# Kernel optimization log

Measured on AMD Instinct MI355X. Metric: run time of the kernel, lower is better.

Reference implementation:

```python
import jax, jax.numpy as jnp
import numpy as np

L, D, F, H, K, V, E = 15, 512, 2048, 64, 128, 30, 1024
DH = D // H  # 8
B, N = 8, 128


def _ln(x, s, b, eps=1e-5):
    m = x.mean(-1, keepdims=True)
    v = ((x - m) ** 2).mean(-1, keepdims=True)
    return (x - m) * jax.lax.rsqrt(v + eps) * s + b


def _gauss(x, mean, std):
    # matches torch.jit gaussian(): pi = 3.14159
    a = (2.0 * 3.14159) ** 0.5
    return jnp.exp(-0.5 * ((x - mean) / std) ** 2) / (a * std)


def setup_inputs() -> dict:
    key = jax.random.key(0)
    ks = iter(jax.random.split(key, 48))
    nrm = lambda shape, sc=0.02: jax.random.normal(next(ks), shape, jnp.float32) * sc
    zeros = lambda shape: jnp.zeros(shape, jnp.float32)
    ones = lambda shape: jnp.ones(shape, jnp.float32)
    return dict(
        src_tokens=jax.random.randint(next(ks), (B, N), 0, V),
        src_distance=jax.random.uniform(next(ks), (B, N, N), jnp.float32) * 3.0,
        src_edge_type=jax.random.randint(next(ks), (B, N, N), 0, E),
        token_embed=nrm((V, D)),
        gbf_means=jax.random.uniform(next(ks), (K,), jnp.float32, 0.0, 3.0),
        gbf_stds=jax.random.uniform(next(ks), (K,), jnp.float32, 0.0, 3.0),
        gbf_mul=ones((E, 1)),
        gbf_bias=zeros((E, 1)),
        proj_w1=nrm((K, K)), proj_b1=zeros((K,)),
        proj_w2=nrm((K, H)), proj_b2=zeros((H,)),
        emb_ln_s=ones((D,)), emb_ln_b=zeros((D,)),
        Wq=nrm((L, D, D)), bq=zeros((L, D)),
        Wk=nrm((L, D, D)), bk=zeros((L, D)),
        Wv=nrm((L, D, D)), bv=zeros((L, D)),
        Wo=nrm((L, D, D)), bo=zeros((L, D)),
        ln1_s=ones((L, D)), ln1_b=zeros((L, D)),
        ln2_s=ones((L, D)), ln2_b=zeros((L, D)),
        Wf1=nrm((L, D, F)), bf1=zeros((L, F)),
        Wf2=nrm((L, F, D)), bf2=zeros((L, D)),
        fin_ln_s=ones((D,)), fin_ln_b=zeros((D,)),
    )


def reference(src_tokens, src_distance, src_edge_type, token_embed,
              gbf_means, gbf_stds, gbf_mul, gbf_bias,
              proj_w1, proj_b1, proj_w2, proj_b2,
              emb_ln_s, emb_ln_b,
              Wq, bq, Wk, bk, Wv, bv, Wo, bo,
              ln1_s, ln1_b, ln2_s, ln2_b,
              Wf1, bf1, Wf2, bf2, fin_ln_s, fin_ln_b):
    # --- GaussianLayer: per-pair edge-type affine + K-kernel RBF -> [B,N,N,K]
    mul = gbf_mul[src_edge_type]          # [B,N,N,1]
    add = gbf_bias[src_edge_type]         # [B,N,N,1]
    g = mul * src_distance[..., None] + add
    std = jnp.abs(gbf_stds) + 1e-5
    g = _gauss(g, gbf_means, std)         # broadcast [B,N,N,1] vs [K] -> [B,N,N,K]
    # --- gbf_proj (NonLinearHead K->K->H) -> attention bias [B,H,N,N]
    hproj = jax.nn.gelu(g @ proj_w1 + proj_b1, approximate=False)
    bias0 = jnp.transpose(hproj @ proj_w2 + proj_b2, (0, 3, 1, 2))

    x = _ln(token_embed[src_tokens], emb_ln_s, emb_ln_b)  # [B,N,D]
    scale = DH ** -0.5

    def layer(carry, p):
        x, bias = carry
        wq, bq_, wk, bk_, wv, bv_, wo, bo_, s1, b1, s2, b2, wf1, bf1_, wf2, bf2_ = p
        # pre-LN self-attention with additive pair bias
        r = x
        y = _ln(x, s1, b1)
        q = (y @ wq + bq_).reshape(B, N, H, DH) * scale
        k = (y @ wk + bk_).reshape(B, N, H, DH)
        v = (y @ wv + bv_).reshape(B, N, H, DH)
        scores = jnp.einsum('bihd,bjhd->bhij', q, k) + bias  # [B,H,N,N]
        probs = jax.nn.softmax(scores, axis=-1)
        o = jnp.einsum('bhij,bjhd->bihd', probs, v).reshape(B, N, D)
        x = r + (o @ wo + bo_)
        # pre-LN FFN
        r = x
        y = _ln(x, s2, b2)
        y = jax.nn.gelu(y @ wf1 + bf1_, approximate=False) @ wf2 + bf2_
        # UniMol: pre-softmax scores feed the next layer as its pair bias
        return (r + y, scores), None

    (x, _), _ = jax.lax.scan(
        layer, (x, bias0),
        (Wq, bq, Wk, bk, Wv, bv, Wo, bo, ln1_s, ln1_b, ln2_s, ln2_b, Wf1, bf1, Wf2, bf2))
    return _ln(x, fin_ln_s, fin_ln_b)  # [B,N,D]
```

## Files before the change

kernel.cpp:

```cpp
#include <hip/hip_runtime.h>
#include <hip/hip_bf16.h>

#define Bv 8
#define Nv 128
#define Dv 512
#define Hv 64
#define DHv 8
#define Fv 2048
#define Lv 15
#define Kv 128

typedef unsigned short u16;
typedef __attribute__((ext_vector_type(8))) short s16x8;
typedef __attribute__((ext_vector_type(4))) float f32x4;

__device__ __forceinline__ float b2f(u16 u) {
    union { unsigned int i; float f; } w;
    w.i = ((unsigned int)u) << 16;
    return w.f;
}

__device__ __forceinline__ u16 f2b(float f) {
    __hip_bfloat16 h = __float2bfloat16(f);
    u16 u;
    __builtin_memcpy(&u, &h, 2);
    return u;
}

__device__ __forceinline__ bool probe_bf16(const void* p) {
    return ((const u16*)p)[0] == 0x3F80u;
}

__device__ __forceinline__ float ldv(const u16* p, size_t i)   { return b2f(p[i]); }
__device__ __forceinline__ float ldv(const float* p, size_t i) { return p[i]; }

__device__ __forceinline__ u16 ld16(const u16* p, size_t i)   { return p[i]; }
__device__ __forceinline__ u16 ld16(const float* p, size_t i) { return f2b(p[i]); }

__device__ __forceinline__ float geluf(float v) {
    return 0.5f * v * (1.0f + erff(v * 0.70710678118654752f));
}

template<typename T>
__device__ __forceinline__ void gbf2_body(
    const T* dist, const int* etype, const T* means, const T* stds,
    const T* mulW, const T* addW, const T* w1, const T* b1w,
    const T* w2, const T* b2w, float* biasOut,
    float* xs, float* smean, float* sinv, u16* GA, u16* Bst)
{
    const int t = threadIdx.x;
    const int iq = blockIdx.x;
    const int j0 = blockIdx.y << 6;
    const int b = blockIdx.z;

    if (t < 64) {
        size_t pidx = ((size_t)(b * Nv + iq)) * Nv + j0 + t;
        int e = etype[pidx];
        xs[t] = ldv(dist, pidx) * ldv(mulW, e) + ldv(addW, e);
    } else if (t >= 128) {
        int k = t - 128;
        float sv = fabsf(ldv(stds, k)) + 1e-5f;
        smean[k] = ldv(means, k);
        sinv[k] = 1.0f / sv;
    }
    __syncthreads();

    {
        const int row = t & 63;
        const int kc = t >> 6;
        const float x = xs[row];
        const int mt = row >> 4, r = row & 15;
        #pragma unroll
        for (int lg2 = 0; lg2 < 4; lg2++) {
            union { s16x8 v; u16 u[8]; } pk;
            #pragma unroll
            for (int j = 0; j < 8; j++) {
                int k = kc * 32 + lg2 * 8 + j;
                float z = (x - smean[k]) * sinv[k];
                pk.u[j] = f2b(expf(-0.5f * z * z) * (0.39894261f * sinv[k]));
            }
            *reinterpret_cast<s16x8*>(&GA[(((mt * 4 + kc) * 4 + lg2) * 16 + r) << 3]) = pk.v;
        }
    }

    const int w = t >> 6, l = t & 63;
    const int lg = l >> 4, lr = l & 15;
    const int wm = (w >> 1) << 5;
    const int wn1 = (w & 1) << 6;
    const int mt0 = wm >> 4;

    const int b1col = t & 127, b1lg0 = (t >> 7) << 1;

    f32x4 acc1[2][4];
    #pragma unroll
    for (int mi = 0; mi < 2; mi++)
        #pragma unroll
        for (int ni = 0; ni < 4; ni++) acc1[mi][ni] = (f32x4){0.f, 0.f, 0.f, 0.f};

    for (int kc = 0; kc < 4; kc++) {
        #pragma unroll
        for (int q = 0; q < 2; q++) {
            int lgq = b1lg0 + q;
            union { s16x8 v; u16 u[8]; } pb;
            #pragma unroll
            for (int j = 0; j < 8; j++)
                pb.u[j] = ld16(w1, (size_t)(kc * 32 + lgq * 8 + j) * Kv + b1col);
            *reinterpret_cast<s16x8*>(
                &Bst[((((b1col >> 4) * 4 + lgq) * 16 + (b1col & 15)) << 3)]) = pb.v;
        }
        __syncthreads();
        s16x8 a0 = *reinterpret_cast<const s16x8*>(&GA[((((mt0 + 0) * 4 + kc) * 4 + lg) * 16 + lr) << 3]);
        s16x8 a1 = *reinterpret_cast<const s16x8*>(&GA[((((mt0 + 1) * 4 + kc) * 4 + lg) * 16 + lr) << 3]);
        #pragma unroll
        for (int ni = 0; ni < 4; ni++) {
            int nt = (wn1 >> 4) + ni;
            s16x8 bf = *reinterpret_cast<const s16x8*>(&Bst[((nt * 4 + lg) * 16 + lr) << 3]);
            acc1[0][ni] = __builtin_amdgcn_mfma_f32_16x16x32_bf16(a0, bf, acc1[0][ni], 0, 0, 0);
            acc1[1][ni] = __builtin_amdgcn_mfma_f32_16x16x32_bf16(a1, bf, acc1[1][ni], 0, 0, 0);
        }
        __syncthreads();
    }

    #pragma unroll
    for (int mi = 0; mi < 2; mi++) {
        #pragma unroll
        for (int ni = 0; ni < 4; ni++) {
            int col = wn1 + ni * 16 + lr;
            float bb = ldv(b1w, col);
            #pragma unroll
            for (int i = 0; i < 4; i++) {
                int row = wm + mi * 16 + lg * 4 + i;
                float v = geluf(acc1[mi][ni][i] + bb);
                GA[((((row >> 4) * 4 + (col >> 5)) * 4 + ((col >> 3) & 3)) * 16 + (row & 15)) * 8 + (col & 7)] = f2b(v);
            }
        }
    }
    __syncthreads();

    const int wn2 = (w & 1) << 5;
    const int b2col = t & 63, b2lg = t >> 6;

    f32x4 acc2[2][2];
    #pragma unroll
    for (int mi = 0; mi < 2; mi++)
        #pragma unroll
        for (int ni = 0; ni < 2; ni++) acc2[mi][ni] = (f32x4){0.f, 0.f, 0.f, 0.f};

    for (int kc = 0; kc < 4; kc++) {
        {
            union { s16x8 v; u16 u[8]; } pb;
            #pragma unroll
            for (int j = 0; j < 8; j++)
                pb.u[j] = ld16(w2, (size_t)(kc * 32 + b2lg * 8 + j) * Hv + b2col);
            *reinterpret_cast<s16x8*>(
                &Bst[((((b2col >> 4) * 4 + b2lg) * 16 + (b2col & 15)) << 3)]) = pb.v;
        }
        __syncthreads();
        s16x8 a0 = *reinterpret_cast<const s16x8*>(&GA[((((mt0 + 0) * 4 + kc) * 4 + lg) * 16 + lr) << 3]);
        s16x8 a1 = *reinterpret_cast<const s16x8*>(&GA[((((mt0 + 1) * 4 + kc) * 4 + lg) * 16 + lr) << 3]);
        #pragma unroll
        for (int ni = 0; ni < 2; ni++) {
            int nt = (wn2 >> 4) + ni;
            s16x8 bf = *reinterpret_cast<const s16x8*>(&Bst[((nt * 4 + lg) * 16 + lr) << 3]);
            acc2[0][ni] = __builtin_amdgcn_mfma_f32_16x16x32_bf16(a0, bf, acc2[0][ni], 0, 0, 0);
            acc2[1][ni] = __builtin_amdgcn_mfma_f32_16x16x32_bf16(a1, bf, acc2[1][ni], 0, 0, 0);
        }
        __syncthreads();
    }

    #pragma unroll
    for (int mi = 0; mi < 2; mi++) {
        #pragma unroll
        for (int ni = 0; ni < 2; ni++) {
            int h = wn2 + ni * 16 + lr;
            int jb = wm + mi * 16 + lg * 4;
            float badd = ldv(b2w, h);
            size_t oidx = (((size_t)(b * Hv + h)) * Nv + iq) * Nv + j0 + jb;
            *reinterpret_cast<float4*>(&biasOut[oidx]) =
                make_float4(acc2[mi][ni][0] + badd, acc2[mi][ni][1] + badd,
                            acc2[mi][ni][2] + badd, acc2[mi][ni][3] + badd);
        }
    }
}

__global__ __launch_bounds__(256) void gbf2_k(
    const void* dist, const int* etype, const void* means, const void* stds,
    const void* mulW, const void* addW, const void* w1, const void* b1,
    const void* w2, const void* b2, float* biasOut, const void* probe)
{
    __shared__ float xs[64];
    __shared__ float smean[Kv];
    __shared__ float sinv[Kv];
    __shared__ __align__(16) u16 GA[8192];
    __shared__ __align__(16) u16 Bst[4096];
    if (probe_bf16(probe))
        gbf2_body<u16>((const u16*)dist, etype, (const u16*)means, (const u16*)stds,
                       (const u16*)mulW, (const u16*)addW, (const u16*)w1, (const u16*)b1,
                       (const u16*)w2, (const u16*)b2, biasOut, xs, smean, sinv, GA, Bst);
    else
        gbf2_body<float>((const float*)dist, etype, (const float*)means, (const float*)stds,
                         (const float*)mulW, (const float*)addW, (const float*)w1, (const float*)b1,
                         (const float*)w2, (const float*)b2, biasOut, xs, smean, sinv, GA, Bst);
}

__device__ __forceinline__ void block_stats_512(float x0, float x1, float& mean, float& rstd)
{
    float sum = x0 + x1, sq = x0 * x0 + x1 * x1;
    #pragma unroll
    for (int off = 32; off; off >>= 1) {
        sum += __shfl_xor(sum, off);
        sq  += __shfl_xor(sq, off);
    }
    __shared__ float ssum[4], ssq[4];
    int t = threadIdx.x;
    if ((t & 63) == 0) { ssum[t >> 6] = sum; ssq[t >> 6] = sq; }
    __syncthreads();
    sum = ssum[0] + ssum[1] + ssum[2] + ssum[3];
    sq  = ssq[0] + ssq[1] + ssq[2] + ssq[3];
    mean = sum * (1.0f / 512.0f);
    float var = sq * (1.0f / 512.0f) - mean * mean;
    rstd = rsqrtf(var + 1e-5f);
}

template<typename T>
__device__ __forceinline__ void embed_body(
    const int* toks, const T* emb, const T* sc, const T* bi, float* xout)
{
    int row = blockIdx.x, t = threadIdx.x;
    int tok = toks[row];
    float x0 = ldv(emb, (size_t)tok * Dv + t);
    float x1 = ldv(emb, (size_t)tok * Dv + t + 256);
    float mean, rstd;
    block_stats_512(x0, x1, mean, rstd);
    xout[(size_t)row * Dv + t]       = (x0 - mean) * rstd * ldv(sc, t) + ldv(bi, t);
    xout[(size_t)row * Dv + t + 256] = (x1 - mean) * rstd * ldv(sc, t + 256) + ldv(bi, t + 256);
}

__global__ __launch_bounds__(256) void embed_ln_k(
    const int* toks, const void* emb, const void* sc, const void* bi,
    float* xout, const void* probe)
{
    if (probe_bf16(probe))
        embed_body<u16>(toks, (const u16*)emb, (const u16*)sc, (const u16*)bi, xout);
    else
        embed_body<float>(toks, (const float*)emb, (const float*)sc, (const float*)bi, xout);
}

template<typename T>
__device__ __forceinline__ void ln_body(
    const float* xin, const T* sc, const T* bi, size_t pofs, float* yout)
{
    int row = blockIdx.x, t = threadIdx.x;
    const float* xp = xin + (size_t)row * Dv;
    float x0 = xp[t], x1 = xp[t + 256];
    float mean, rstd;
    block_stats_512(x0, x1, mean, rstd);
    yout[(size_t)row * Dv + t]       = (x0 - mean) * rstd * ldv(sc, pofs + t) + ldv(bi, pofs + t);
    yout[(size_t)row * Dv + t + 256] = (x1 - mean) * rstd * ldv(sc, pofs + t + 256) + ldv(bi, pofs + t + 256);
}

__global__ __launch_bounds__(256) void ln_k(
    const float* xin, const void* sc, const void* bi, unsigned long long pofs,
    float* yout, const void* probe)
{
    if (probe_bf16(probe))
        ln_body<u16>(xin, (const u16*)sc, (const u16*)bi, (size_t)pofs, yout);
    else
        ln_body<float>(xin, (const float*)sc, (const float*)bi, (size_t)pofs, yout);
}

template<typename T, bool OUT_BF>
__device__ __forceinline__ void final_ln_body(
    const float* xin, const T* sc, const T* bi, void* yout)
{
    int row = blockIdx.x, t = threadIdx.x;
    const float* xp = xin + (size_t)row * Dv;
    float x0 = xp[t], x1 = xp[t + 256];
    float mean, rstd;
    block_stats_512(x0, x1, mean, rstd);
    float o0 = (x0 - mean) * rstd * ldv(sc, t) + ldv(bi, t);
    float o1 = (x1 - mean) * rstd * ldv(sc, t + 256) + ldv(bi, t + 256);
    if (OUT_BF) {
        __hip_bfloat16* yp = (__hip_bfloat16*)yout;
        yp[(size_t)row * Dv + t]       = __float2bfloat16(o0);
        yp[(size_t)row * Dv + t + 256] = __float2bfloat16(o1);
    } else {
        float* yp = (float*)yout;
        yp[(size_t)row * Dv + t]       = o0;
        yp[(size_t)row * Dv + t + 256] = o1;
    }
}

__global__ __launch_bounds__(256) void final_ln_k(
    const float* xin, const void* sc, const void* bi, void* yout, const void* probe)
{
    if (probe_bf16(probe))
        final_ln_body<u16, true>(xin, (const u16*)sc, (const u16*)bi, yout);
    else
        final_ln_body<float, false>(xin, (const float*)sc, (const float*)bi, yout);
}

template<typename T>
__device__ __forceinline__ void gemm_mfma_body(
    const float* A, const T* W, const T* bias, const float* R,
    float* C, int Nc, int Kc, int act, int res, int kbegin, int kend, int raw,
    u16* Al, u16* Bl)
{
    const int tid = threadIdx.x;
    const int l = tid & 63, w = tid >> 6;
    const int wm = (w >> 1) << 5, wn = (w & 1) << 5;
    const int bm = blockIdx.y * 64, bn = blockIdx.x * 64;
    const int lg = l >> 4, lr = l & 15;
    const int mt0 = wm >> 4, nt0 = wn >> 4;

    f32x4 acc00 = {}, acc01 = {}, acc10 = {}, acc11 = {};

    const int arow = tid >> 2, akq = tid & 3;
    const float* aGp = A + (size_t)(bm + arow) * Kc + (akq << 3);
    const int aL0 = ((((arow >> 4) * 2 + 0) * 4 + akq) * 16 + (arow & 15)) << 3;
    const int aL1 = ((((arow >> 4) * 2 + 1) * 4 + akq) * 16 + (arow & 15)) << 3;

    const int bcol = tid & 63;
    const int be = tid >> 6;
    const int bc = be >> 1, blg0 = (be & 1) << 1;
    const int bnt = bcol >> 4, bcl = bcol & 15;

    for (int kt = kbegin; kt < kend; kt += 64) {
        {
            float4 a0 = *reinterpret_cast<const float4*>(aGp + kt);
            float4 a1 = *reinterpret_cast<const float4*>(aGp + kt + 4);
            float4 a2 = *reinterpret_cast<const float4*>(aGp + kt + 32);
            float4 a3 = *reinterpret_cast<const float4*>(aGp + kt + 36);
            union { s16x8 v; u16 u[8]; } p0, p1;
            p0.u[0] = f2b(a0.x); p0.u[1] = f2b(a0.y); p0.u[2] = f2b(a0.z); p0.u[3] = f2b(a0.w);
            p0.u[4] = f2b(a1.x); p0.u[5] = f2b(a1.y); p0.u[6] = f2b(a1.z); p0.u[7] = f2b(a1.w);
            p1.u[0] = f2b(a2.x); p1.u[1] = f2b(a2.y); p1.u[2] = f2b(a2.z); p1.u[3] = f2b(a2.w);
            p1.u[4] = f2b(a3.x); p1.u[5] = f2b(a3.y); p1.u[6] = f2b(a3.z); p1.u[7] = f2b(a3.w);
            *reinterpret_cast<s16x8*>(&Al[aL0]) = p0.v;
            *reinterpret_cast<s16x8*>(&Al[aL1]) = p1.v;
        }
        #pragma unroll
        for (int q = 0; q < 2; q++) {
            int lgq = blg0 + q;
            union { s16x8 v; u16 u[8]; } pb;
            #pragma unroll
            for (int j = 0; j < 8; j++)
                pb.u[j] = ld16(W, (size_t)(kt + bc * 32 + lgq * 8 + j) * Nc + bn + bcol);
            *reinterpret_cast<s16x8*>(
                &Bl[(((bnt * 2 + bc) * 4 + lgq) * 16 + bcl) << 3]) = pb.v;
        }
        __syncthreads();
        #pragma unroll
        for (int c = 0; c < 2; c++) {
            s16x8 af0 = *reinterpret_cast<const s16x8*>(&Al[((((mt0 + 0) * 2 + c) * 4 + lg) * 16 + lr) << 3]);
            s16x8 af1 = *reinterpret_cast<const s16x8*>(&Al[((((mt0 + 1) * 2 + c) * 4 + lg) * 16 + lr) << 3]);
            s16x8 bf0 = *reinterpret_cast<const s16x8*>(&Bl[((((nt0 + 0) * 2 + c) * 4 + lg) * 16 + lr) << 3]);
            s16x8 bf1 = *reinterpret_cast<const s16x8*>(&Bl[((((nt0 + 1) * 2 + c) * 4 + lg) * 16 + lr) << 3]);
            acc00 = __builtin_amdgcn_mfma_f32_16x16x32_bf16(af0, bf0, acc00, 0, 0, 0);
            acc01 = __builtin_amdgcn_mfma_f32_16x16x32_bf16(af0, bf1, acc01, 0, 0, 0);
            acc10 = __builtin_amdgcn_mfma_f32_16x16x32_bf16(af1, bf0, acc10, 0, 0, 0);
            acc11 = __builtin_amdgcn_mfma_f32_16x16x32_bf16(af1, bf1, acc11, 0, 0, 0);
        }
        __syncthreads();
    }

    #pragma unroll
    for (int mi = 0; mi < 2; mi++) {
        #pragma unroll
        for (int i = 0; i < 4; i++) {
            const int row = bm + wm + mi * 16 + lg * 4 + i;
            float* Crow = C + (size_t)row * Nc;
            const float* Rrow = res ? (R + (size_t)row * Nc) : nullptr;
            #pragma unroll
            for (int ni = 0; ni < 2; ni++) {
                const int col = bn + wn + ni * 16 + lr;
                float cv = (ni == 0) ? (mi == 0 ? acc00[i] : acc10[i])
                                     : (mi == 0 ? acc01[i] : acc11[i]);
                if (!raw) {
                    cv += ldv(bias, col);
                    if (act) cv = geluf(cv);
                    if (res) cv += Rrow[col];
                }
                Crow[col] = cv;
            }
        }
    }
}

__global__ __launch_bounds__(256) void gemm_k(
    const float* A, const void* W, unsigned long long wofs,
    const void* bias, unsigned long long bofs, const float* R,
    float* C, int Nc, int Kc, int act, int res, const void* probe)
{
    __shared__ __align__(16) u16 Al[4096];
    __shared__ __align__(16) u16 Bl[4096];
    const int nz = gridDim.z, z = blockIdx.z;
    const int kchunk = Kc / nz;
    const int kbegin = z * kchunk, kend = kbegin + kchunk;
    const int raw = (nz > 1) ? 1 : 0;
    float* Cz = C + (size_t)z * ((size_t)gridDim.y * 64) * Nc;
    if (probe_bf16(probe))
        gemm_mfma_body<u16>(A, (const u16*)W + wofs, (const u16*)bias + bofs, R, Cz,
                            Nc, Kc, act, res, kbegin, kend, raw, Al, Bl);
    else
        gemm_mfma_body<float>(A, (const float*)W + wofs, (const float*)bias + bofs, R, Cz,
                              Nc, Kc, act, res, kbegin, kend, raw, Al, Bl);
}

__global__ __launch_bounds__(256) void qkv_k(
    const float* A,
    const void* W0, const void* W1p, const void* W2p, unsigned long long wofs,
    const void* b0, const void* b1p, const void* b2p, unsigned long long bofs,
    float* C0, float* C1, float* C2, const void* probe)
{
    __shared__ __align__(16) u16 Al[4096];
    __shared__ __align__(16) u16 Bl[4096];
    const int z = blockIdx.z;
    const void* W  = (z == 0) ? W0 : (z == 1) ? W1p : W2p;
    const void* bb = (z == 0) ? b0 : (z == 1) ? b1p : b2p;
    float* C       = (z == 0) ? C0 : (z == 1) ? C1 : C2;
    if (probe_bf16(probe))
        gemm_mfma_body<u16>(A, (const u16*)W + wofs, (const u16*)bb + bofs, nullptr, C,
                            Dv, Dv, 0, 0, 0, Dv, 0, Al, Bl);
    else
        gemm_mfma_body<float>(A, (const float*)W + wofs, (const float*)bb + bofs, nullptr, C,
                              Dv, Dv, 0, 0, 0, Dv, 0, Al, Bl);
}

template<typename T>
__device__ __forceinline__ void combln_body(
    const float* parts, const T* pbias, float* X,
    const T* lnS, const T* lnB, size_t pofs, float* Y)
{
    const int t = threadIdx.x;
    const int rowb = t >> 7;
    const int col = (t & 127) << 2;
    const int row = (blockIdx.x << 1) + rowb;
    const size_t idx = (size_t)row * Dv + col;

    float4 sv = *reinterpret_cast<const float4*>(&parts[idx]);
    #pragma unroll
    for (int p = 1; p < 4; p++) {
        const float4 q2 = *reinterpret_cast<const float4*>(&parts[(size_t)p * 524288 + idx]);
        sv.x += q2.x; sv.y += q2.y; sv.z += q2.z; sv.w += q2.w;
    }
    sv.x += ldv(pbias, col);     sv.y += ldv(pbias, col + 1);
    sv.z += ldv(pbias, col + 2); sv.w += ldv(pbias, col + 3);
    const float4 r = *reinterpret_cast<const float4*>(&X[idx]);
    sv.x += r.x; sv.y += r.y; sv.z += r.z; sv.w += r.w;
    *reinterpret_cast<float4*>(&X[idx]) = sv;

    float sum = sv.x + sv.y + sv.z + sv.w;
    float sq  = sv.x * sv.x + sv.y * sv.y + sv.z * sv.z + sv.w * sv.w;
    #pragma unroll
    for (int off = 32; off; off >>= 1) {
        sum += __shfl_xor(sum, off);
        sq  += __shfl_xor(sq, off);
    }
    __shared__ float ssum[4], ssq[4];
    const int wv = t >> 6;
    if ((t & 63) == 0) { ssum[wv] = sum; ssq[wv] = sq; }
    __syncthreads();
    sum = ssum[rowb * 2] + ssum[rowb * 2 + 1];
    sq  = ssq[rowb * 2] + ssq[rowb * 2 + 1];
    const float mean = sum * (1.0f / 512.0f);
    const float var = sq * (1.0f / 512.0f) - mean * mean;
    const float rstd = rsqrtf(var + 1e-5f);

    float4 yv;
    yv.x = (sv.x - mean) * rstd * ldv(lnS, pofs + col)     + ldv(lnB, pofs + col);
    yv.y = (sv.y - mean) * rstd * ldv(lnS, pofs + col + 1) + ldv(lnB, pofs + col + 1);
    yv.z = (sv.z - mean) * rstd * ldv(lnS, pofs + col + 2) + ldv(lnB, pofs + col + 2);
    yv.w = (sv.w - mean) * rstd * ldv(lnS, pofs + col + 3) + ldv(lnB, pofs + col + 3);
    *reinterpret_cast<float4*>(&Y[idx]) = yv;
}

__global__ __launch_bounds__(256) void combln_k(
    const float* parts, const void* pbias, unsigned long long bofs, float* X,
    const void* lnS, const void* lnB, unsigned long long pofs, float* Y,
    const void* probe)
{
    if (probe_bf16(probe))
        combln_body<u16>(parts, (const u16*)pbias + bofs, X,
                         (const u16*)lnS, (const u16*)lnB, (size_t)pofs, Y);
    else
        combln_body<float>(parts, (const float*)pbias + bofs, X,
                           (const float*)lnS, (const float*)lnB, (size_t)pofs, Y);
}

__global__ __launch_bounds__(512) void attn_k(
    const float* __restrict__ q, const float* __restrict__ k, const float* __restrict__ v,
    float* bias, float* __restrict__ o)
{
    __shared__ __align__(16) float ks[Nv][DHv];
    __shared__ __align__(16) float vs[Nv][DHv];

    const int t = threadIdx.x;
    const int h = blockIdx.x;
    const int b = blockIdx.y;
    const int i = (blockIdx.z << 6) + (t >> 3);
    const int e = t & 7;
    const float scale = 0.35355339059327373f;

    const float* kh = k + (size_t)(b * Nv) * Dv + h * DHv;
    const float* vh = v + (size_t)(b * Nv) * Dv + h * DHv;

    {
        const int j = t >> 2, c = (t & 3) << 1;
        const float2 k2 = *reinterpret_cast<const float2*>(kh + (size_t)j * Dv + c);
        const float2 v2 = *reinterpret_cast<const float2*>(vh + (size_t)j * Dv + c);
        *reinterpret_cast<float2*>(&ks[j][c]) = k2;
        *reinterpret_cast<float2*>(&vs[j][c]) = v2;
    }

    const float* qp = q + (size_t)(b * Nv + i) * Dv + h * DHv;
    const float4 q0 = *reinterpret_cast<const float4*>(qp);
    const float4 q1 = *reinterpret_cast<const float4*>(qp + 4);

    float* bp = bias + (((size_t)(b * Hv + h)) * Nv + i) * Nv;

    float s[16];
    #pragma unroll
    for (int w = 0; w < 16; w++) s[w] = bp[(w << 3) + e];

    __syncthreads();

    float mx = -1e30f;
    #pragma unroll
    for (int w = 0; w < 16; w++) {
        const int j = (w << 3) + e;
        const float4 k0 = *reinterpret_cast<const float4*>(&ks[j][0]);
        const float4 k1 = *reinterpret_cast<const float4*>(&ks[j][4]);
        float d = q0.x * k0.x + q0.y * k0.y + q0.z * k0.z + q0.w * k0.w +
                  q1.x * k1.x + q1.y * k1.y + q1.z * k1.z + q1.w * k1.w;
        float val = s[w] + scale * d;
        s[w] = val;
        bp[j] = val;
        mx = fmaxf(mx, val);
    }

    mx = fmaxf(mx, __shfl_xor(mx, 1));
    mx = fmaxf(mx, __shfl_xor(mx, 2));
    mx = fmaxf(mx, __shfl_xor(mx, 4));

    float sum = 0.0f;
    #pragma unroll
    for (int w = 0; w < 16; w++) {
        s[w] = expf(s[w] - mx);
        sum += s[w];
    }
    sum += __shfl_xor(sum, 1);
    sum += __shfl_xor(sum, 2);
    sum += __shfl_xor(sum, 4);
    const float inv = 1.0f / sum;

    float a0 = 0, a1 = 0, a2 = 0, a3 = 0, a4 = 0, a5 = 0, a6 = 0, a7 = 0;
    #pragma unroll
    for (int w = 0; w < 16; w++) {
        const int j = (w << 3) + e;
        const float4 v0 = *reinterpret_cast<const float4*>(&vs[j][0]);
        const float4 v1 = *reinterpret_cast<const float4*>(&vs[j][4]);
        const float p = s[w];
        a0 += p * v0.x; a1 += p * v0.y; a2 += p * v0.z; a3 += p * v0.w;
        a4 += p * v1.x; a5 += p * v1.y; a6 += p * v1.z; a7 += p * v1.w;
    }
    a0 += __shfl_xor(a0, 1); a0 += __shfl_xor(a0, 2); a0 += __shfl_xor(a0, 4);
    a1 += __shfl_xor(a1, 1); a1 += __shfl_xor(a1, 2); a1 += __shfl_xor(a1, 4);
    a2 += __shfl_xor(a2, 1); a2 += __shfl_xor(a2, 2); a2 += __shfl_xor(a2, 4);
    a3 += __shfl_xor(a3, 1); a3 += __shfl_xor(a3, 2); a3 += __shfl_xor(a3, 4);
    a4 += __shfl_xor(a4, 1); a4 += __shfl_xor(a4, 2); a4 += __shfl_xor(a4, 4);
    a5 += __shfl_xor(a5, 1); a5 += __shfl_xor(a5, 2); a5 += __shfl_xor(a5, 4);
    a6 += __shfl_xor(a6, 1); a6 += __shfl_xor(a6, 2); a6 += __shfl_xor(a6, 4);
    a7 += __shfl_xor(a7, 1); a7 += __shfl_xor(a7, 2); a7 += __shfl_xor(a7, 4);

    if (e == 0) {
        float* op = o + (size_t)(b * Nv + i) * Dv + h * DHv;
        *reinterpret_cast<float4*>(op)     = make_float4(a0 * inv, a1 * inv, a2 * inv, a3 * inv);
        *reinterpret_cast<float4*>(op + 4) = make_float4(a4 * inv, a5 * inv, a6 * inv, a7 * inv);
    }
}

extern "C" void kernel_launch(void* const* d_in, const int* in_sizes, int n_in,
                              void* d_out, int out_size, void* d_ws, size_t ws_size,
                              hipStream_t stream)
{
    const int*  src_tokens = (const int*)d_in[0];
    const void* src_dist   = d_in[1];
    const int*  src_edge   = (const int*)d_in[2];
    const void* token_emb  = d_in[3];
    const void* gbf_means  = d_in[4];
    const void* gbf_stds   = d_in[5];
    const void* gbf_mul    = d_in[6];
    const void* gbf_bias   = d_in[7];
    const void* pw1        = d_in[8];
    const void* pb1        = d_in[9];
    const void* pw2        = d_in[10];
    const void* pb2        = d_in[11];
    const void* embs       = d_in[12];
    const void* embb       = d_in[13];
    const void* Wq         = d_in[14];
    const void* bq         = d_in[15];
    const void* Wk         = d_in[16];
    const void* bk         = d_in[17];
    const void* Wv         = d_in[18];
    const void* bvp        = d_in[19];
    const void* Wo         = d_in[20];
    const void* bo         = d_in[21];
    const void* ln1s       = d_in[22];
    const void* ln1b       = d_in[23];
    const void* ln2s       = d_in[24];
    const void* ln2b       = d_in[25];
    const void* Wf1        = d_in[26];
    const void* bf1        = d_in[27];
    const void* Wf2        = d_in[28];
    const void* bf2        = d_in[29];
    const void* fins       = d_in[30];
    const void* finb       = d_in[31];
    const void* probe      = embs;

    float* ws   = (float*)d_ws;
    float* x    = ws;
    float* y    = x  + 524288;
    float* qb   = y  + 524288;
    float* kb   = qb + 524288;
    float* vb   = kb + 524288;
    float* ob   = vb + 524288;
    float* hb   = ob + 524288;
    float* bias = hb + 2097152;

    gbf2_k<<<dim3(Nv, 2, Bv), 256, 0, stream>>>(
        src_dist, src_edge, gbf_means, gbf_stds, gbf_mul, gbf_bias,
        pw1, pb1, pw2, pb2, bias, probe);
    embed_ln_k<<<Bv * Nv, 256, 0, stream>>>(src_tokens, token_emb, embs, embb, x, probe);
    ln_k<<<Bv * Nv, 256, 0, stream>>>(x, ln1s, ln1b, 0ull, y, probe);

    dim3 gQKV(512 / 64, 1024 / 64, 3);
    dim3 gS4(512 / 64, 1024 / 64, 4);
    dim3 gF1(2048 / 64, 1024 / 64);
    for (int l = 0; l < Lv; l++) {
        unsigned long long wofs  = (unsigned long long)l * Dv * Dv;
        unsigned long long wofsF = (unsigned long long)l * Dv * Fv;
        unsigned long long dof   = (unsigned long long)l * Dv;
        unsigned long long fof   = (unsigned long long)l * Fv;
        unsigned long long nofs  = (l + 1 < Lv) ? (unsigned long long)(l + 1) * Dv : 0ull;

        qkv_k<<<gQKV, 256, 0, stream>>>(y, Wq, Wk, Wv, wofs, bq, bk, bvp, dof,
                                        qb, kb, vb, probe);
        attn_k<<<dim3(Hv, Bv, 2), 512, 0, stream>>>(qb, kb, vb, bias, ob);
        gemm_k<<<gS4, 256, 0, stream>>>(ob, Wo, wofs, bo, dof, nullptr, y, 512, 512, 0, 0, probe);
        combln_k<<<512, 256, 0, stream>>>(y, bo, dof, x, ln2s, ln2b, dof, y, probe);
        gemm_k<<<gF1, 256, 0, stream>>>(y, Wf1, wofsF, bf1, fof, nullptr, hb, 2048, 512, 1, 0, probe);
        gemm_k<<<gS4, 256, 0, stream>>>(hb, Wf2, wofsF, bf2, fof, nullptr, y, 512, 2048, 0, 0, probe);
        combln_k<<<512, 256, 0, stream>>>(y, bf2, dof, x, ln1s, ln1b, nofs, y, probe);
    }
    final_ln_k<<<Bv * Nv, 256, 0, stream>>>(x, fins, finb, d_out, probe);
}
```

Before: 1.470 ms.

## Store GEMM activations in bf16 and prefetch next K tile into registers

Layernorm, combine-layernorm, attention output and the FFN1 GELU output are now written as bf16, so GEMMs load bf16 A tiles directly instead of loading fp32 and converting. The GEMM main loop also prefetches the next K tile of A and W into registers while the current tile is computed from shared memory. This halves activation traffic and removes per-tile conversions, and the prefetch overlaps global load latency with MFMA work. The cost is extra register pressure and rounding of the FFN hidden state to bf16 before FFN2, which previously happened inside the GEMM anyway.

New measurement: 1.471 ms. No clear change (+0.0%).

```diff
diff --git a/kernel.cpp b/kernel.cpp
--- a/kernel.cpp
+++ b/kernel.cpp
@@ -248,20 +248,20 @@
 
 template<typename T>
 __device__ __forceinline__ void ln_body(
-    const float* xin, const T* sc, const T* bi, size_t pofs, float* yout)
+    const float* xin, const T* sc, const T* bi, size_t pofs, u16* yout)
 {
     int row = blockIdx.x, t = threadIdx.x;
     const float* xp = xin + (size_t)row * Dv;
     float x0 = xp[t], x1 = xp[t + 256];
     float mean, rstd;
     block_stats_512(x0, x1, mean, rstd);
-    yout[(size_t)row * Dv + t]       = (x0 - mean) * rstd * ldv(sc, pofs + t) + ldv(bi, pofs + t);
-    yout[(size_t)row * Dv + t + 256] = (x1 - mean) * rstd * ldv(sc, pofs + t + 256) + ldv(bi, pofs + t + 256);
+    yout[(size_t)row * Dv + t]       = f2b((x0 - mean) * rstd * ldv(sc, pofs + t) + ldv(bi, pofs + t));
+    yout[(size_t)row * Dv + t + 256] = f2b((x1 - mean) * rstd * ldv(sc, pofs + t + 256) + ldv(bi, pofs + t + 256));
 }
 
 __global__ __launch_bounds__(256) void ln_k(
     const float* xin, const void* sc, const void* bi, unsigned long long pofs,
-    float* yout, const void* probe)
+    u16* yout, const void* probe)
 {
     if (probe_bf16(probe))
         ln_body<u16>(xin, (const u16*)sc, (const u16*)bi, (size_t)pofs, yout);
@@ -302,9 +302,9 @@
 
 template<typename T>
 __device__ __forceinline__ void gemm_mfma_body(
-    const float* A, const T* W, const T* bias, const float* R,
-    float* C, int Nc, int Kc, int act, int res, int kbegin, int kend, int raw,
-    u16* Al, u16* Bl)
+    const u16* A, const T* W, const T* bias, const float* R,
+    void* C, int Nc, int Kc, int act, int res, int kbegin, int kend,
+    int raw, int cbf, u16* Al, u16* Bl)
 {
     const int tid = threadIdx.x;
     const int l = tid & 63, w = tid >> 6;
@@ -316,7 +316,7 @@
     f32x4 acc00 = {}, acc01 = {}, acc10 = {}, acc11 = {};
 
     const int arow = tid >> 2, akq = tid & 3;
-    const float* aGp = A + (size_t)(bm + arow) * Kc + (akq << 3);
+    const u16* aGp = A + (size_t)(bm + arow) * Kc + (akq << 3);
     const int aL0 = ((((arow >> 4) * 2 + 0) * 4 + akq) * 16 + (arow & 15)) << 3;
     const int aL1 = ((((arow >> 4) * 2 + 1) * 4 + akq) * 16 + (arow & 15)) << 3;
 
@@ -324,32 +324,42 @@
     const int be = tid >> 6;
     const int bc = be >> 1, blg0 = (be & 1) << 1;
     const int bnt = bcol >> 4, bcl = bcol & 15;
+    const int bL0 = (((bnt * 2 + bc) * 4 + blg0) * 16 + bcl) << 3;
+    const int bL1 = (((bnt * 2 + bc) * 4 + blg0 + 1) * 16 + bcl) << 3;
+
+    s16x8 ra0, ra1, rb0, rb1;
+    ra0 = *reinterpret_cast<const s16x8*>(aGp + kbegin);
+    ra1 = *reinterpret_cast<const s16x8*>(aGp + kbegin + 32);
+    {
+        union { s16x8 v; u16 u[8]; } p0, p1;
+        #pragma unroll
+        for (int j = 0; j < 8; j++) {
+            p0.u[j] = ld16(W, (size_t)(kbegin + bc * 32 + blg0 * 8 + j) * Nc + bn + bcol);
+            p1.u[j] = ld16(W, (size_t)(kbegin + bc * 32 + blg0 * 8 + 8 + j) * Nc + bn + bcol);
+        }
+        rb0 = p0.v; rb1 = p1.v;
+    }
 
     for (int kt = kbegin; kt < kend; kt += 64) {
-        {
-            float4 a0 = *reinterpret_cast<const float4*>(aGp + kt);
-            float4 a1 = *reinterpret_cast<const float4*>(aGp + kt + 4);
-            float4 a2 = *reinterpret_cast<const float4*>(aGp + kt + 32);
-            float4 a3 = *reinterpret_cast<const float4*>(aGp + kt + 36);
+        *reinterpret_cast<s16x8*>(&Al[aL0]) = ra0;
+        *reinterpret_cast<s16x8*>(&Al[aL1]) = ra1;
+        *reinterpret_cast<s16x8*>(&Bl[bL0]) = rb0;
+        *reinterpret_cast<s16x8*>(&Bl[bL1]) = rb1;
+        __syncthreads();
+
+        const int kn = kt + 64;
+        if (kn < kend) {
+            ra0 = *reinterpret_cast<const s16x8*>(aGp + kn);
+            ra1 = *reinterpret_cast<const s16x8*>(aGp + kn + 32);
             union { s16x8 v; u16 u[8]; } p0, p1;
-            p0.u[0] = f2b(a0.x); p0.u[1] = f2b(a0.y); p0.u[2] = f2b(a0.z); p0.u[3] = f2b(a0.w);
-            p0.u[4] = f2b(a1.x); p0.u[5] = f2b(a1.y); p0.u[6] = f2b(a1.z); p0.u[7] = f2b(a1.w);
-            p1.u[0] = f2b(a2.x); p1.u[1] = f2b(a2.y); p1.u[2] = f2b(a2.z); p1.u[3] = f2b(a2.w);
-            p1.u[4] = f2b(a3.x); p1.u[5] = f2b(a3.y); p1.u[6] = f2b(a3.z); p1.u[7] = f2b(a3.w);
-            *reinterpret_cast<s16x8*>(&Al[aL0]) = p0.v;
-            *reinterpret_cast<s16x8*>(&Al[aL1]) = p1.v;
-        }
-        #pragma unroll
-        for (int q = 0; q < 2; q++) {
-            int lgq = blg0 + q;
-            union { s16x8 v; u16 u[8]; } pb;
             #pragma unroll
-            for (int j = 0; j < 8; j++)
-                pb.u[j] = ld16(W, (size_t)(kt + bc * 32 + lgq * 8 + j) * Nc + bn + bcol);
-            *reinterpret_cast<s16x8*>(
-                &Bl[(((bnt * 2 + bc) * 4 + lgq) * 16 + bcl) << 3]) = pb.v;
-        }
-        __syncthreads();
+            for (int j = 0; j < 8; j++) {
+                p0.u[j] = ld16(W, (size_t)(kn + bc * 32 + blg0 * 8 + j) * Nc + bn + bcol);
+                p1.u[j] = ld16(W, (size_t)(kn + bc * 32 + blg0 * 8 + 8 + j) * Nc + bn + bcol);
+            }
+            rb0 = p0.v; rb1 = p1.v;
+        }
+
         #pragma unroll
         for (int c = 0; c < 2; c++) {
             s16x8 af0 = *reinterpret_cast<const s16x8*>(&Al[((((mt0 + 0) * 2 + c) * 4 + lg) * 16 + lr) << 3]);
@@ -369,28 +379,30 @@
         #pragma unroll
         for (int i = 0; i < 4; i++) {
             const int row = bm + wm + mi * 16 + lg * 4 + i;
-            float* Crow = C + (size_t)row * Nc;
             const float* Rrow = res ? (R + (size_t)row * Nc) : nullptr;
             #pragma unroll
             for (int ni = 0; ni < 2; ni++) {
                 const int col = bn + wn + ni * 16 + lr;
                 float cv = (ni == 0) ? (mi == 0 ? acc00[i] : acc10[i])
                                      : (mi == 0 ? acc01[i] : acc11[i]);
-                if (!raw) {
+                if (raw) {
+                    ((float*)C)[(size_t)row * Nc + col] = cv;
+                } else {
                     cv += ldv(bias, col);
                     if (act) cv = geluf(cv);
                     if (res) cv += Rrow[col];
+                    if (cbf) ((u16*)C)[(size_t)row * Nc + col] = f2b(cv);
+                    else     ((float*)C)[(size_t)row * Nc + col] = cv;
                 }
-                Crow[col] = cv;
             }
         }
     }
 }
 
 __global__ __launch_bounds__(256) void gemm_k(
-    const float* A, const void* W, unsigned long long wofs,
+    const u16* A, const void* W, unsigned long long wofs,
     const void* bias, unsigned long long bofs, const float* R,
-    float* C, int Nc, int Kc, int act, int res, const void* probe)
+    void* C, int Nc, int Kc, int act, int res, int cbf, const void* probe)
 {
     __shared__ __align__(16) u16 Al[4096];
     __shared__ __align__(16) u16 Bl[4096];
@@ -398,17 +410,17 @@
     const int kchunk = Kc / nz;
     const int kbegin = z * kchunk, kend = kbegin + kchunk;
     const int raw = (nz > 1) ? 1 : 0;
-    float* Cz = C + (size_t)z * ((size_t)gridDim.y * 64) * Nc;
+    void* Cz = (char*)C + (size_t)z * ((size_t)gridDim.y * 64) * Nc * sizeof(float);
     if (probe_bf16(probe))
         gemm_mfma_body<u16>(A, (const u16*)W + wofs, (const u16*)bias + bofs, R, Cz,
-                            Nc, Kc, act, res, kbegin, kend, raw, Al, Bl);
+                            Nc, Kc, act, res, kbegin, kend, raw, cbf, Al, Bl);
     else
         gemm_mfma_body<float>(A, (const float*)W + wofs, (const float*)bias + bofs, R, Cz,
-                              Nc, Kc, act, res, kbegin, kend, raw, Al, Bl);
+                              Nc, Kc, act, res, kbegin, kend, raw, cbf, Al, Bl);
 }
 
 __global__ __launch_bounds__(256) void qkv_k(
-    const float* A,
+    const u16* A,
     const void* W0, const void* W1p, const void* W2p, unsigned long long wofs,
     const void* b0, const void* b1p, const void* b2p, unsigned long long bofs,
     float* C0, float* C1, float* C2, const void* probe)
@@ -421,16 +433,16 @@
     float* C       = (z == 0) ? C0 : (z == 1) ? C1 : C2;
     if (probe_bf16(probe))
         gemm_mfma_body<u16>(A, (const u16*)W + wofs, (const u16*)bb + bofs, nullptr, C,
-                            Dv, Dv, 0, 0, 0, Dv, 0, Al, Bl);
+                            Dv, Dv, 0, 0, 0, Dv, 0, 0, Al, Bl);
     else
         gemm_mfma_body<float>(A, (const float*)W + wofs, (const float*)bb + bofs, nullptr, C,
-                              Dv, Dv, 0, 0, 0, Dv, 0, Al, Bl);
+                              Dv, Dv, 0, 0, 0, Dv, 0, 0, Al, Bl);
 }
 
 template<typename T>
 __device__ __forceinline__ void combln_body(
     const float* parts, const T* pbias, float* X,
-    const T* lnS, const T* lnB, size_t pofs, float* Y)
+    const T* lnS, const T* lnB, size_t pofs, u16* Y)
 {
     const int t = threadIdx.x;
     const int rowb = t >> 7;
@@ -467,17 +479,17 @@
     const float var = sq * (1.0f / 512.0f) - mean * mean;
     const float rstd = rsqrtf(var + 1e-5f);
 
-    float4 yv;
-    yv.x = (sv.x - mean) * rstd * ldv(lnS, pofs + col)     + ldv(lnB, pofs + col);
-    yv.y = (sv.y - mean) * rstd * ldv(lnS, pofs + col + 1) + ldv(lnB, pofs + col + 1);
-    yv.z = (sv.z - mean) * rstd * ldv(lnS, pofs + col + 2) + ldv(lnB, pofs + col + 2);
-    yv.w = (sv.w - mean) * rstd * ldv(lnS, pofs + col + 3) + ldv(lnB, pofs + col + 3);
-    *reinterpret_cast<float4*>(&Y[idx]) = yv;
+    ushort4 yv;
+    yv.x = f2b((sv.x - mean) * rstd * ldv(lnS, pofs + col)     + ldv(lnB, pofs + col));
+    yv.y = f2b((sv.y - mean) * rstd * ldv(lnS, pofs + col + 1) + ldv(lnB, pofs + col + 1));
+    yv.z = f2b((sv.z - mean) * rstd * ldv(lnS, pofs + col + 2) + ldv(lnB, pofs + col + 2));
+    yv.w = f2b((sv.w - mean) * rstd * ldv(lnS, pofs + col + 3) + ldv(lnB, pofs + col + 3));
+    *reinterpret_cast<ushort4*>(&Y[idx]) = yv;
 }
 
 __global__ __launch_bounds__(256) void combln_k(
     const float* parts, const void* pbias, unsigned long long bofs, float* X,
-    const void* lnS, const void* lnB, unsigned long long pofs, float* Y,
+    const void* lnS, const void* lnB, unsigned long long pofs, u16* Y,
     const void* probe)
 {
     if (probe_bf16(probe))
@@ -490,7 +502,7 @@
 
 __global__ __launch_bounds__(512) void attn_k(
     const float* __restrict__ q, const float* __restrict__ k, const float* __restrict__ v,
-    float* bias, float* __restrict__ o)
+    float* bias, u16* __restrict__ o)
 {
     __shared__ __align__(16) float ks[Nv][DHv];
     __shared__ __align__(16) float vs[Nv][DHv];
@@ -574,9 +586,11 @@
     a7 += __shfl_xor(a7, 1); a7 += __shfl_xor(a7, 2); a7 += __shfl_xor(a7, 4);
 
     if (e == 0) {
-        float* op = o + (size_t)(b * Nv + i) * Dv + h * DHv;
-        *reinterpret_cast<float4*>(op)     = make_float4(a0 * inv, a1 * inv, a2 * inv, a3 * inv);
-        *reinterpret_cast<float4*>(op + 4) = make_float4(a4 * inv, a5 * inv, a6 * inv, a7 * inv);
+        u16* op = o + (size_t)(b * Nv + i) * Dv + h * DHv;
+        ushort4 o0 = { f2b(a0 * inv), f2b(a1 * inv), f2b(a2 * inv), f2b(a3 * inv) };
+        ushort4 o1 = { f2b(a4 * inv), f2b(a5 * inv), f2b(a6 * inv), f2b(a7 * inv) };
+        *reinterpret_cast<ushort4*>(op)     = o0;
+        *reinterpret_cast<ushort4*>(op + 4) = o1;
     }
 }
 
@@ -626,13 +640,16 @@
     float* vb   = kb + 524288;
     float* ob   = vb + 524288;
     float* hb   = ob + 524288;
+    u16*   hbf  = (u16*)hb;
+    u16*   ybf  = (u16*)(hb + 1048576);
+    u16*   obf  = (u16*)(hb + 1310720);
     float* bias = hb + 2097152;
 
     gbf2_k<<<dim3(Nv, 2, Bv), 256, 0, stream>>>(
         src_dist, src_edge, gbf_means, gbf_stds, gbf_mul, gbf_bias,
         pw1, pb1, pw2, pb2, bias, probe);
     embed_ln_k<<<Bv * Nv, 256, 0, stream>>>(src_tokens, token_emb, embs, embb, x, probe);
-    ln_k<<<Bv * Nv, 256, 0, stream>>>(x, ln1s, ln1b, 0ull, y, probe);
+    ln_k<<<Bv * Nv, 256, 0, stream>>>(x, ln1s, ln1b, 0ull, ybf, probe);
 
     dim3 gQKV(512 / 64, 1024 / 64, 3);
     dim3 gS4(512 / 64, 1024 / 64, 4);
@@ -644,14 +661,14 @@
         unsigned long long fof   = (unsigned long long)l * Fv;
         unsigned long long nofs  = (l + 1 < Lv) ? (unsigned long long)(l + 1) * Dv : 0ull;
 
-        qkv_k<<<gQKV, 256, 0, stream>>>(y, Wq, Wk, Wv, wofs, bq, bk, bvp, dof,
+        qkv_k<<<gQKV, 256, 0, stream>>>(ybf, Wq, Wk, Wv, wofs, bq, bk, bvp, dof,
                                         qb, kb, vb, probe);
-        attn_k<<<dim3(Hv, Bv, 2), 512, 0, stream>>>(qb, kb, vb, bias, ob);
-        gemm_k<<<gS4, 256, 0, stream>>>(ob, Wo, wofs, bo, dof, nullptr, y, 512, 512, 0, 0, probe);
-        combln_k<<<512, 256, 0, stream>>>(y, bo, dof, x, ln2s, ln2b, dof, y, probe);
-        gemm_k<<<gF1, 256, 0, stream>>>(y, Wf1, wofsF, bf1, fof, nullptr, hb, 2048, 512, 1, 0, probe);
-        gemm_k<<<gS4, 256, 0, stream>>>(hb, Wf2, wofsF, bf2, fof, nullptr, y, 512, 2048, 0, 0, probe);
-        combln_k<<<512, 256, 0, stream>>>(y, bf2, dof, x, ln1s, ln1b, nofs, y, probe);
+        attn_k<<<dim3(Hv, Bv, 2), 512, 0, stream>>>(qb, kb, vb, bias, obf);
+        gemm_k<<<gS4, 256, 0, stream>>>(obf, Wo, wofs, bo, dof, nullptr, y, 512, 512, 0, 0, 0, probe);
+        combln_k<<<512, 256, 0, stream>>>(y, bo, dof, x, ln2s, ln2b, dof, ybf, probe);
+        gemm_k<<<gF1, 256, 0, stream>>>(ybf, Wf1, wofsF, bf1, fof, nullptr, hbf, 2048, 512, 1, 0, 1, probe);
+        gemm_k<<<gS4, 256, 0, stream>>>(hbf, Wf2, wofsF, bf2, fof, nullptr, y, 512, 2048, 0, 0, 0, probe);
+        combln_k<<<512, 256, 0, stream>>>(y, bf2, dof, x, ln1s, ln1b, nofs, ybf, probe);
     }
     final_ln_k<<<Bv * Nv, 256, 0, stream>>>(x, fins, finb, d_out, probe);
 }
```
